# Optimization experiments

Hardware: AMD Instinct MI355X
Metric: run time of the kernel (lower is better)

The kernel has to match this reference:

```python
import jax, jax.numpy as jnp
import numpy as np

RECON_W = 0.1
CONT_W = 0.2
EPS = 1e-7  # BCE log clamp (torch clamps log at -100; eps-clip is the jax analogue)


def setup_inputs() -> dict:
    key = jax.random.key(0)
    k1, k2, k3, k4 = jax.random.split(key, 4)
    B, M = 256, 4096
    predictions = jax.random.uniform(k1, (B, M, 9), dtype=jnp.float32)
    targets = jax.random.uniform(k2, (B, M, 9), dtype=jnp.float32)
    reconstructed = jax.random.normal(k3, (B, 1, 128, 128), dtype=jnp.float32)
    images = jax.random.normal(k4, (B, 1, 128, 128), dtype=jnp.float32)
    return {"predictions": predictions, "targets": targets,
            "reconstructed": reconstructed, "images": images}


def _continuity_loss(p3, valid_mask):
    # p3: [B, M, 2]; valid_mask: [B, M] bool
    # For each valid slot i, find the next valid slot j > i and accumulate
    # mean(|p3[i] - p3[j]|) -- vectorized replacement for the ragged double loop.
    B, M, _ = p3.shape
    idx = jnp.arange(M, dtype=jnp.int32)
    BIG = jnp.int32(M)
    pos = jnp.where(valid_mask, idx[None, :], BIG)              # [B, M]
    # suffix min over j >= i of pos, then shift to get strict j > i
    suf = jnp.flip(jax.lax.cummin(jnp.flip(pos, axis=1), axis=1), axis=1)
    nxt = jnp.concatenate([suf[:, 1:], jnp.full((B, 1), BIG, jnp.int32)], axis=1)
    pair_valid = valid_mask & (nxt < BIG)                       # [B, M]
    nxt_c = jnp.clip(nxt, 0, M - 1)
    p3_next = jnp.take_along_axis(p3, nxt_c[..., None], axis=1)  # [B, M, 2]
    dist = jnp.abs(p3 - p3_next).mean(axis=-1)                  # [B, M]
    return jnp.sum(dist * pair_valid.astype(p3.dtype)) / B


def _loss(predictions, targets, reconstructed, images):
    target_curves = targets[..., :8]
    target_validity = targets[..., 8:9]
    valid_mask = target_validity[..., 0] > 0.5                  # [B, M]
    fmask = valid_mask.astype(predictions.dtype)
    n_valid = jnp.sum(fmask)

    def masked_l1(pred, tgt, width):
        num = jnp.sum(jnp.abs(pred - tgt) * fmask[..., None])
        return jnp.where(n_valid > 0, num / jnp.maximum(n_valid * width, 1.0), 0.0)

    coord_loss = masked_l1(predictions[..., :6], target_curves[..., :6], 6.0)
    width_loss = masked_l1(predictions[..., 6:8], target_curves[..., 6:8], 2.0)

    p = jnp.clip(predictions[..., 8:9], EPS, 1.0 - EPS)
    t = target_validity
    validity_loss = jnp.mean(-(t * jnp.log(p) + (1.0 - t) * jnp.log(1.0 - p)))

    continuity_loss = _continuity_loss(predictions[..., 4:6], valid_mask)
    reconstruction_loss = jnp.mean((reconstructed - images) ** 2)

    total = (coord_loss + width_loss + 2.0 * validity_loss
             + CONT_W * continuity_loss + RECON_W * reconstruction_loss)
    return total


def reference(predictions, targets, reconstructed, images):
    return _loss(predictions, targets, reconstructed, images)
```

## Files before the change

### kernel.cpp

```cpp
#include <hip/hip_runtime.h>
#include <math.h>

#define B_DIM 256
#define M_DIM 4096
#define EPSV 1e-7f
#define THREADS 1024
#define CHUNK 1024
#define CHUNK_F4 (CHUNK * 9 / 4)
#define NCHUNK (M_DIM / CHUNK)
#define ROW_F4 (M_DIM * 9 / 4)
#define RECON_F4_PER_BLOCK ((B_DIM * 128 * 128 / 4) / B_DIM)
#define TAIL (CHUNK_F4 - 2 * THREADS)


#define LOADC(cc, P0, P1, P2, T0, T1, T2)                      \
    do {                                                       \
        const float4* pc_ = pb + (cc) * CHUNK_F4;              \
        const float4* tc_ = tb + (cc) * CHUNK_F4;              \
        P0 = pc_[t];        T0 = tc_[t];                       \
        P1 = pc_[t + 1024]; T1 = tc_[t + 1024];                \
        if (t < TAIL) { P2 = pc_[t + 2048]; T2 = tc_[t + 2048]; } \
    } while (0)

#define STOREC(P0, P1, P2, T0, T1, T2)                         \
    do {                                                       \
        ((float4*)s_pred)[t]        = P0;                      \
        ((float4*)s_tgt)[t]         = T0;                      \
        ((float4*)s_pred)[t + 1024] = P1;                      \
        ((float4*)s_tgt)[t + 1024]  = T1;                      \
        if (t < TAIL) {                                        \
            ((float4*)s_pred)[t + 2048] = P2;                  \
            ((float4*)s_tgt)[t + 2048]  = T2;                  \
        }                                                      \
    } while (0)

__global__ void __launch_bounds__(THREADS)
__attribute__((amdgpu_waves_per_eu(4, 4)))
fused_loss_kernel(
    const float4* __restrict__ pred4, const float4* __restrict__ tgt4,
    const float4* __restrict__ rec4, const float4* __restrict__ img4,
    float* __restrict__ blk_out)
{
    __shared__ float s_pred[CHUNK * 9];
    __shared__ float s_tgt[CHUNK * 9];
    __shared__ float s_p4[M_DIM];
    __shared__ float s_p5[M_DIM];
    __shared__ unsigned long long s_words[M_DIM / 64];
    __shared__ float s_red[16][6];

    const int b    = blockIdx.x;
    const int t    = threadIdx.x;
    const int lane = t & 63;
    const int wave = t >> 6;

    const float4* pb = pred4 + (size_t)b * ROW_F4;
    const float4* tb = tgt4  + (size_t)b * ROW_F4;

    float coord_s = 0.f, width_s = 0.f, val_s = 0.f, nval_s = 0.f;

    auto consume = [&](int c) {
        const float* pe = s_pred + t * 9;
        const float* te = s_tgt  + t * 9;
        float p0 = pe[0], p1 = pe[1], p2 = pe[2], p3 = pe[3], p4 = pe[4],
              p5 = pe[5], p6 = pe[6], p7 = pe[7], p8 = pe[8];
        float t0 = te[0], t1 = te[1], t2 = te[2], t3 = te[3], t4 = te[4],
              t5 = te[5], t6 = te[6], t7 = te[7], t8 = te[8];

        bool valid = (t8 > 0.5f);
        float fm = valid ? 1.f : 0.f;
        coord_s += fm * (fabsf(p0 - t0) + fabsf(p1 - t1) + fabsf(p2 - t2) +
                         fabsf(p3 - t3) + fabsf(p4 - t4) + fabsf(p5 - t5));
        width_s += fm * (fabsf(p6 - t6) + fabsf(p7 - t7));
        nval_s  += fm;

        float pc8 = fminf(fmaxf(p8, EPSV), 1.0f - EPSV);
        val_s += -(t8 * __logf(pc8) + (1.0f - t8) * __logf(1.0f - pc8));

        const int m = c * CHUNK + t;
        s_p4[m] = p4;
        s_p5[m] = p5;
        unsigned long long bal = __ballot(valid);
        if (lane == 0) s_words[c * 16 + wave] = bal;
    };

    float4 PA0, PA1, PA2, TA0, TA1, TA2;
    float4 PB0, PB1, PB2, TB0, TB1, TB2;

    LOADC(0, PA0, PA1, PA2, TA0, TA1, TA2);

    float recon_s = 0.f;
    {
        const float4* rb = rec4 + (size_t)b * RECON_F4_PER_BLOCK;
        const float4* ib = img4 + (size_t)b * RECON_F4_PER_BLOCK;
        #pragma unroll
        for (int i = 0; i < RECON_F4_PER_BLOCK / THREADS; ++i) {
            int idx = i * THREADS + t;
            float4 r = rb[idx]; float4 m = ib[idx];
            float d0 = r.x - m.x, d1 = r.y - m.y, d2 = r.z - m.z, d3 = r.w - m.w;
            recon_s += d0 * d0 + d1 * d1 + d2 * d2 + d3 * d3;
        }
    }

    STOREC(PA0, PA1, PA2, TA0, TA1, TA2);
    __syncthreads();
    LOADC(1, PB0, PB1, PB2, TB0, TB1, TB2);
    consume(0);

    __syncthreads();
    STOREC(PB0, PB1, PB2, TB0, TB1, TB2);
    __syncthreads();
    LOADC(2, PA0, PA1, PA2, TA0, TA1, TA2);
    consume(1);

    __syncthreads();
    STOREC(PA0, PA1, PA2, TA0, TA1, TA2);
    __syncthreads();
    LOADC(3, PB0, PB1, PB2, TB0, TB1, TB2);
    consume(2);

    __syncthreads();
    STOREC(PB0, PB1, PB2, TB0, TB1, TB2);
    __syncthreads();
    consume(3);

    __syncthreads();

    float cont_s = 0.f;
    #pragma unroll
    for (int p = 0; p < 4; ++p) {
        const int m   = p * 1024 + t;
        const int w   = m >> 6;
        const int bit = m & 63;
        unsigned long long wv = s_words[w];
        if ((wv >> bit) & 1ULL) {
            unsigned long long mask = wv & ((bit == 63) ? 0ULL : (~0ULL << (bit + 1)));
            int nxt = -1;
            if (mask) {
                nxt = (w << 6) + __builtin_ctzll(mask);
            } else {
                for (int w2 = w + 1; w2 < (M_DIM / 64); ++w2) {
                    unsigned long long mw = s_words[w2];
                    if (mw) { nxt = (w2 << 6) + __builtin_ctzll(mw); break; }
                }
            }
            if (nxt >= 0) {
                cont_s += 0.5f * (fabsf(s_p4[m] - s_p4[nxt]) +
                                  fabsf(s_p5[m] - s_p5[nxt]));
            }
        }
    }

    float vals[6] = {coord_s, width_s, val_s, nval_s, cont_s, recon_s};
    #pragma unroll
    for (int i = 0; i < 6; ++i) {
        float v = vals[i];
        #pragma unroll
        for (int off = 32; off > 0; off >>= 1) v += __shfl_down(v, off, 64);
        vals[i] = v;
    }
    if (lane == 0) {
        #pragma unroll
        for (int i = 0; i < 6; ++i) s_red[wave][i] = vals[i];
    }
    __syncthreads();
    if (t == 0) {
        float acc[6] = {0.f, 0.f, 0.f, 0.f, 0.f, 0.f};
        for (int wv = 0; wv < 16; ++wv)
            #pragma unroll
            for (int i = 0; i < 6; ++i) acc[i] += s_red[wv][i];
        float* r = blk_out + b * 8;
        #pragma unroll
        for (int i = 0; i < 6; ++i) r[i] = acc[i];
    }
}

__global__ __launch_bounds__(256) void finalize_kernel(
    const float* __restrict__ ws, float* __restrict__ out)
{
    const int t = threadIdx.x;
    const float* rb = ws + t * 8;
    float v[6];
    #pragma unroll
    for (int i = 0; i < 6; ++i) v[i] = rb[i];

    __shared__ float sred[4][6];
    int lane = t & 63, wave = t >> 6;
    #pragma unroll
    for (int i = 0; i < 6; ++i) {
        float x = v[i];
        #pragma unroll
        for (int off = 32; off > 0; off >>= 1) x += __shfl_down(x, off, 64);
        v[i] = x;
    }
    if (lane == 0)
        #pragma unroll
        for (int i = 0; i < 6; ++i) sred[wave][i] = v[i];
    __syncthreads();
    if (t == 0) {
        double a[6];
        #pragma unroll
        for (int i = 0; i < 6; ++i)
            a[i] = (double)sred[0][i] + (double)sred[1][i] +
                   (double)sred[2][i] + (double)sred[3][i];
        double coord_num = a[0], width_num = a[1], val_sum = a[2],
               nv = a[3], cont = a[4], recon = a[5];

        double coord = (nv > 0.0) ? coord_num / fmax(nv * 6.0, 1.0) : 0.0;
        double width = (nv > 0.0) ? width_num / fmax(nv * 2.0, 1.0) : 0.0;
        double validity = val_sum / ((double)B_DIM * (double)M_DIM);
        double contl    = cont / (double)B_DIM;
        double reconl   = recon / ((double)B_DIM * 128.0 * 128.0);

        out[0] = (float)(coord + width + 2.0 * validity +
                         0.2 * contl + 0.1 * reconl);
    }
}

extern "C" void kernel_launch(void* const* d_in, const int* in_sizes, int n_in,
                              void* d_out, int out_size, void* d_ws, size_t ws_size,
                              hipStream_t stream) {
    const float* pred = (const float*)d_in[0];
    const float* tgt  = (const float*)d_in[1];
    const float* rec  = (const float*)d_in[2];
    const float* img  = (const float*)d_in[3];
    float* ws = (float*)d_ws;

    fused_loss_kernel<<<B_DIM, THREADS, 0, stream>>>(
        (const float4*)pred, (const float4*)tgt,
        (const float4*)rec, (const float4*)img, ws);
    finalize_kernel<<<1, 256, 0, stream>>>(ws, (float*)d_out);
}
```

Measured before the change: 131.2 us.

## Stage pred/target per wave to drop block-wide barriers in load pipeline

Each wave now owns a contiguous 256-element slice of the row and stages it through a private LDS buffer in 64-element sub-chunks. All __syncthreads inside the double-buffered load/consume pipeline are removed, so waves progress independently. Validity bit words are indexed per wave slice to keep global ordering. It relies on intra-wave lockstep for LDS ordering, and per-wave global loads are shorter contiguous runs.

```diff
diff --git a/kernel.cpp b/kernel.cpp
--- a/kernel.cpp
+++ b/kernel.cpp
@@ -5,33 +5,32 @@
 #define M_DIM 4096
 #define EPSV 1e-7f
 #define THREADS 1024
-#define CHUNK 1024
-#define CHUNK_F4 (CHUNK * 9 / 4)
-#define NCHUNK (M_DIM / CHUNK)
+#define NWAVES (THREADS / 64)
+#define WAVE_ELEMS (M_DIM / NWAVES)
+#define SUB 64
+#define NSUB (WAVE_ELEMS / SUB)
+#define SUB_F4 (SUB * 9 / 4)
+#define WAVE_F4 (WAVE_ELEMS * 9 / 4)
 #define ROW_F4 (M_DIM * 9 / 4)
 #define RECON_F4_PER_BLOCK ((B_DIM * 128 * 128 / 4) / B_DIM)
-#define TAIL (CHUNK_F4 - 2 * THREADS)
-
-
-#define LOADC(cc, P0, P1, P2, T0, T1, T2)                      \
-    do {                                                       \
-        const float4* pc_ = pb + (cc) * CHUNK_F4;              \
-        const float4* tc_ = tb + (cc) * CHUNK_F4;              \
-        P0 = pc_[t];        T0 = tc_[t];                       \
-        P1 = pc_[t + 1024]; T1 = tc_[t + 1024];                \
-        if (t < TAIL) { P2 = pc_[t + 2048]; T2 = tc_[t + 2048]; } \
+
+
+#define LOADW(cc, P0, P1, P2, T0, T1, T2)                              \
+    do {                                                               \
+        const float4* pc_ = pw + (cc) * SUB_F4;                        \
+        const float4* tc_ = tw + (cc) * SUB_F4;                        \
+        P0 = pc_[lane];      T0 = tc_[lane];                           \
+        P1 = pc_[lane + 64]; T1 = tc_[lane + 64];                      \
+        if (lane < 16) { P2 = pc_[lane + 128]; T2 = tc_[lane + 128]; } \
     } while (0)
 
-#define STOREC(P0, P1, P2, T0, T1, T2)                         \
-    do {                                                       \
-        ((float4*)s_pred)[t]        = P0;                      \
-        ((float4*)s_tgt)[t]         = T0;                      \
-        ((float4*)s_pred)[t + 1024] = P1;                      \
-        ((float4*)s_tgt)[t + 1024]  = T1;                      \
-        if (t < TAIL) {                                        \
-            ((float4*)s_pred)[t + 2048] = P2;                  \
-            ((float4*)s_tgt)[t + 2048]  = T2;                  \
-        }                                                      \
+#define STOREW(P0, P1, P2, T0, T1, T2)                                 \
+    do {                                                               \
+        float4* sp_ = (float4*)(s_stage[wave]);                        \
+        float4* st_ = (float4*)(s_stage[wave] + 576);                  \
+        sp_[lane] = P0;      st_[lane] = T0;                           \
+        sp_[lane + 64] = P1; st_[lane + 64] = T1;                      \
+        if (lane < 16) { sp_[lane + 128] = P2; st_[lane + 128] = T2; } \
     } while (0)
 
 __global__ void __launch_bounds__(THREADS)
@@ -41,8 +40,7 @@
     const float4* __restrict__ rec4, const float4* __restrict__ img4,
     float* __restrict__ blk_out)
 {
-    __shared__ float s_pred[CHUNK * 9];
-    __shared__ float s_tgt[CHUNK * 9];
+    __shared__ float s_stage[NWAVES][1152];
     __shared__ float s_p4[M_DIM];
     __shared__ float s_p5[M_DIM];
     __shared__ unsigned long long s_words[M_DIM / 64];
@@ -53,14 +51,14 @@
     const int lane = t & 63;
     const int wave = t >> 6;
 
-    const float4* pb = pred4 + (size_t)b * ROW_F4;
-    const float4* tb = tgt4  + (size_t)b * ROW_F4;
+    const float4* pw = pred4 + (size_t)b * ROW_F4 + wave * WAVE_F4;
+    const float4* tw = tgt4  + (size_t)b * ROW_F4 + wave * WAVE_F4;
 
     float coord_s = 0.f, width_s = 0.f, val_s = 0.f, nval_s = 0.f;
 
     auto consume = [&](int c) {
-        const float* pe = s_pred + t * 9;
-        const float* te = s_tgt  + t * 9;
+        const float* pe = s_stage[wave] + lane * 9;
+        const float* te = s_stage[wave] + 576 + lane * 9;
         float p0 = pe[0], p1 = pe[1], p2 = pe[2], p3 = pe[3], p4 = pe[4],
               p5 = pe[5], p6 = pe[6], p7 = pe[7], p8 = pe[8];
         float t0 = te[0], t1 = te[1], t2 = te[2], t3 = te[3], t4 = te[4],
@@ -76,17 +74,17 @@
         float pc8 = fminf(fmaxf(p8, EPSV), 1.0f - EPSV);
         val_s += -(t8 * __logf(pc8) + (1.0f - t8) * __logf(1.0f - pc8));
 
-        const int m = c * CHUNK + t;
+        const int m = wave * WAVE_ELEMS + c * SUB + lane;
         s_p4[m] = p4;
         s_p5[m] = p5;
         unsigned long long bal = __ballot(valid);
-        if (lane == 0) s_words[c * 16 + wave] = bal;
+        if (lane == 0) s_words[wave * NSUB + c] = bal;
     };
 
     float4 PA0, PA1, PA2, TA0, TA1, TA2;
     float4 PB0, PB1, PB2, TB0, TB1, TB2;
 
-    LOADC(0, PA0, PA1, PA2, TA0, TA1, TA2);
+    LOADW(0, PA0, PA1, PA2, TA0, TA1, TA2);
 
     float recon_s = 0.f;
     {
@@ -101,26 +99,19 @@
         }
     }
 
-    STOREC(PA0, PA1, PA2, TA0, TA1, TA2);
-    __syncthreads();
-    LOADC(1, PB0, PB1, PB2, TB0, TB1, TB2);
+    STOREW(PA0, PA1, PA2, TA0, TA1, TA2);
+    LOADW(1, PB0, PB1, PB2, TB0, TB1, TB2);
     consume(0);
 
-    __syncthreads();
-    STOREC(PB0, PB1, PB2, TB0, TB1, TB2);
-    __syncthreads();
-    LOADC(2, PA0, PA1, PA2, TA0, TA1, TA2);
+    STOREW(PB0, PB1, PB2, TB0, TB1, TB2);
+    LOADW(2, PA0, PA1, PA2, TA0, TA1, TA2);
     consume(1);
 
-    __syncthreads();
-    STOREC(PA0, PA1, PA2, TA0, TA1, TA2);
-    __syncthreads();
-    LOADC(3, PB0, PB1, PB2, TB0, TB1, TB2);
+    STOREW(PA0, PA1, PA2, TA0, TA1, TA2);
+    LOADW(3, PB0, PB1, PB2, TB0, TB1, TB2);
     consume(2);
 
-    __syncthreads();
-    STOREC(PB0, PB1, PB2, TB0, TB1, TB2);
-    __syncthreads();
+    STOREW(PB0, PB1, PB2, TB0, TB1, TB2);
     consume(3);
 
     __syncthreads();
```

Measured after the change: 132.4 us. Within noise of the previous version (+0.9%).
